# Kernel optimization log

Measured on AMD Instinct MI355X. Metric: run time of the kernel, lower is better.

The kernel has to match this reference:

```python
import jax, jax.numpy as jnp
import numpy as np

N = 50000   # nodes
E = 600000  # edges
D = 128     # embedding_dim
L = 4       # num_message_passing_steps


def setup_inputs() -> dict:
    key = jax.random.key(0)
    ks = jax.random.split(key, 5)
    x = jax.random.normal(ks[0], (N, D), dtype=jnp.float32)
    edge_index = jax.random.randint(ks[1], (2, E), 0, N, dtype=jnp.int32)
    # Per-layer params: MPNN linear (no bias), GCNConv weight + bias.
    lin_w = jax.random.normal(ks[2], (L, D, D), dtype=jnp.float32) / np.sqrt(D).astype(np.float32)
    gcn_w = jax.random.normal(ks[3], (L, D, D), dtype=jnp.float32) / np.sqrt(D).astype(np.float32)
    gcn_b = jax.random.normal(ks[4], (L, D), dtype=jnp.float32) * 0.01
    return {"x": x, "edge_index": edge_index, "lin_w": lin_w, "gcn_w": gcn_w, "gcn_b": gcn_b}


def reference(x, edge_index, lin_w, gcn_w, gcn_b):
    n = x.shape[0]
    # GCNConv defaults: add_self_loops=True, normalize=True.
    loops = jnp.arange(n, dtype=edge_index.dtype)
    src = jnp.concatenate([edge_index[0], loops])  # [E+N]
    dst = jnp.concatenate([edge_index[1], loops])  # [E+N]
    # Degree computed on dst (col) for flow='source_to_target'.
    deg = jax.ops.segment_sum(jnp.ones_like(src, dtype=x.dtype), dst, num_segments=n)
    dinv = jnp.where(deg > 0, jax.lax.rsqrt(jnp.maximum(deg, 1.0)), 0.0)
    norm = dinv[src] * dinv[dst]  # [E+N]

    for l in range(lin_w.shape[0]):
        h = x @ lin_w[l].T                 # MPNNLayer.linear (no bias)
        h = h @ gcn_w[l].T                 # GCNConv internal linear
        msgs = h[src] * norm[:, None]      # gather + normalize  [E+N, D]
        agg = jax.ops.segment_sum(msgs, dst, num_segments=n)
        x = agg + gcn_b[l]                 # GCNConv bias
        # NOTE: self.relu is `Sequential as ReLU` -> empty Sequential = identity.
    return x
```

## Files before the change

kernel.cpp:

```cpp
#include <hip/hip_runtime.h>

#define DEMB 128
#define EB 8192

typedef __attribute__((ext_vector_type(8))) _Float16 half8;
typedef __attribute__((ext_vector_type(4))) _Float16 half4;
typedef __attribute__((ext_vector_type(4))) float f32x4;

__global__ void kwc(const float* __restrict__ gcn, const float* __restrict__ lin,
                    float* __restrict__ Ms) {
  __shared__ float sa[128];
  int l = blockIdx.x >> 7, i = blockIdx.x & 127, j = threadIdx.x;
  sa[j] = gcn[((size_t)l * 128 + i) * 128 + j];
  __syncthreads();
  float acc = 0.f;
#pragma unroll 8
  for (int k = 0; k < 128; ++k) acc += sa[k] * lin[((size_t)l * 128 + k) * 128 + j];
  Ms[((size_t)l * 128 + i) * 128 + j] = acc;
}

__global__ void kst2(const float* __restrict__ Ms, const float* __restrict__ gb,
                     float* __restrict__ A1, float* __restrict__ B1,
                     float* __restrict__ v0, float* __restrict__ cb) {
  const float* M0 = Ms;
  const float* M1 = Ms + 16384;
  const float* M2 = Ms + 2 * 16384;
  const float* M3 = Ms + 3 * 16384;
  __shared__ float sa[128];
  int b = blockIdx.x, j = threadIdx.x;
  if (b < 128) {
    sa[j] = M1[b * 128 + j];
    __syncthreads();
    float acc = 0.f;
#pragma unroll 8
    for (int k = 0; k < 128; ++k) acc += sa[k] * M0[k * 128 + j];
    A1[b * 128 + j] = acc;
  } else if (b < 256) {
    int i = b - 128;
    sa[j] = M3[i * 128 + j];
    __syncthreads();
    float acc = 0.f;
#pragma unroll 8
    for (int k = 0; k < 128; ++k) acc += sa[k] * M2[k * 128 + j];
    B1[i * 128 + j] = acc;
  } else if (b == 256) {
    sa[j] = gb[j];
    __syncthreads();
    float acc = 0.f;
#pragma unroll 8
    for (int k = 0; k < 128; ++k) acc += M1[j * 128 + k] * sa[k];
    v0[j] = acc;
  } else {
    sa[j] = gb[2 * 128 + j];
    __syncthreads();
    float acc = 0.f;
#pragma unroll 8
    for (int k = 0; k < 128; ++k) acc += M3[j * 128 + k] * sa[k];
    cb[256 + j] = acc;
  }
}

__global__ void kst3(const float* __restrict__ A1, const float* __restrict__ B1,
                     const float* __restrict__ v0, const float* __restrict__ gb,
                     _Float16* __restrict__ Rh, float* __restrict__ cb) {
  __shared__ float sa[128];
  int b = blockIdx.x, j = threadIdx.x;
  if (b < 128) {
    sa[j] = B1[b * 128 + j];
    __syncthreads();
    float acc = 0.f;
#pragma unroll 8
    for (int k = 0; k < 128; ++k) acc += sa[k] * A1[k * 128 + j];
    Rh[b * 128 + j] = (_Float16)acc;
  } else if (b == 128) {
    sa[j] = v0[j];
    __syncthreads();
    float acc = 0.f;
#pragma unroll 8
    for (int k = 0; k < 128; ++k) acc += B1[j * 128 + k] * sa[k];
    cb[j] = acc;
  } else {
    sa[j] = gb[128 + j];
    __syncthreads();
    float acc = 0.f;
#pragma unroll 8
    for (int k = 0; k < 128; ++k) acc += B1[j * 128 + k] * sa[k];
    cb[128 + j] = acc;
  }
}

__global__ void khist(const int* __restrict__ ei, int* __restrict__ histG,
                      int etot, int nbB) {
  __shared__ int lh[256];
  int t = threadIdx.x;
  lh[t] = 0;
  __syncthreads();
#pragma unroll 4
  for (int j = 0; j < EB / 256; ++j) {
    int i = blockIdx.x * EB + j * 256 + t;
    if (i < etot) atomicAdd(&lh[ei[etot + i] >> 8], 1);
  }
  __syncthreads();
  histG[t * nbB + blockIdx.x] = lh[t];
}

__global__ void kbase(int* __restrict__ histG, int* __restrict__ binOff,
                      int nbB, int etot) {
  __shared__ int s[256];
  int t = threadIdx.x;
  int* row = histG + t * nbB;
  int tot = 0;
#pragma unroll 4
  for (int b = 0; b < nbB; ++b) tot += row[b];
  s[t] = tot;
  __syncthreads();
  for (int o = 1; o < 256; o <<= 1) {
    int v = (t >= o) ? s[t - o] : 0;
    __syncthreads();
    s[t] += v;
    __syncthreads();
  }
  int bstart = s[t] - tot;
  binOff[t] = bstart;
  if (t == 255) binOff[256] = etot;
  int run = bstart;
  for (int b = 0; b < nbB; ++b) {
    int v = row[b];
    row[b] = run;
    run += v;
  }
}

__global__ void kscatter(const int* __restrict__ ei, const int* __restrict__ histG,
                         int2* __restrict__ pr, int etot, int nbB) {
  __shared__ int cur[256];
  int t = threadIdx.x;
  cur[t] = histG[t * nbB + blockIdx.x];
  __syncthreads();
#pragma unroll 4
  for (int j = 0; j < EB / 256; ++j) {
    int i = blockIdx.x * EB + j * 256 + t;
    if (i < etot) {
      int src = ei[i], dst = ei[etot + i];
      int p = atomicAdd(&cur[dst >> 8], 1);
      pr[p] = make_int2(src, dst);
    }
  }
}

__global__ void kdeg2(const int2* __restrict__ pr, const int* __restrict__ binOff,
                      int* __restrict__ deg, int n) {
  __shared__ int dl[256];
  int t = threadIdx.x, b = blockIdx.x;
  dl[t] = 0;
  __syncthreads();
  int s1 = binOff[b + 1];
  for (int p = binOff[b] + t; p < s1; p += 256)
    atomicAdd(&dl[pr[p].y & 255], 1);
  __syncthreads();
  int node = (b << 8) + t;
  if (node < n) deg[node] = dl[t];
}

__global__ void kscan1(const int* __restrict__ deg, int* __restrict__ off,
                       int* __restrict__ bsum, float* __restrict__ dinv,
                       float* __restrict__ dinv2, int n) {
  __shared__ int s[256];
  int t = threadIdx.x, i = blockIdx.x * 256 + t;
  int c = 0;
  if (i < n) {
    c = deg[i];
    float dv = rsqrtf((float)(c + 1));
    dinv[i] = dv;
    dinv2[i] = dv * dv;
  }
  s[t] = c;
  __syncthreads();
  for (int o = 1; o < 256; o <<= 1) {
    int v = (t >= o) ? s[t - o] : 0;
    __syncthreads();
    s[t] += v;
    __syncthreads();
  }
  if (i < n) off[i] = s[t] - c;
  if (t == 255) bsum[blockIdx.x] = s[t];
}

__global__ void kscan2(const int* __restrict__ bsum, int* __restrict__ boff,
                       int nb, int* __restrict__ off, int n, int etot) {
  __shared__ int s[256];
  int t = threadIdx.x;
  int c = (t < nb) ? bsum[t] : 0;
  s[t] = c;
  __syncthreads();
  for (int o = 1; o < 256; o <<= 1) {
    int v = (t >= o) ? s[t - o] : 0;
    __syncthreads();
    s[t] += v;
    __syncthreads();
  }
  if (t < nb) boff[t] = s[t] - c;
  if (t == 0) off[n] = etot;
}

__global__ void kscan3(int* __restrict__ off, const int* __restrict__ boff, int n) {
  int i = blockIdx.x * 256 + threadIdx.x;
  if (i < n) off[i] += boff[i >> 8];
}

__global__ void kfill2(const int2* __restrict__ pr, const int* __restrict__ binOff,
                       const int* __restrict__ off, int* __restrict__ csr, int n) {
  __shared__ int cur[256];
  int t = threadIdx.x, b = blockIdx.x;
  int node = (b << 8) + t;
  cur[t] = (node < n) ? off[node] : 0;
  __syncthreads();
  int s1 = binOff[b + 1];
  for (int p = binOff[b] + t; p < s1; p += 256) {
    int2 e = pr[p];
    int pos = atomicAdd(&cur[e.y & 255], 1);
    csr[pos] = e.x;
  }
}

__global__ void kpre(const float* __restrict__ x, const float* __restrict__ dinv,
                     _Float16* __restrict__ xh, int n) {
  int gid = blockIdx.x * 256 + threadIdx.x;
  if (gid >= n * 32) return;
  int r = gid >> 5, c = (gid & 31) * 4;
  float d = dinv[r];
  float4 v = *(const float4*)(x + (size_t)r * DEMB + c);
  half4 o = {(_Float16)(v.x * d), (_Float16)(v.y * d), (_Float16)(v.z * d), (_Float16)(v.w * d)};
  *(half4*)(xh + (size_t)r * DEMB + c) = o;
}

template <int WITHU>
__launch_bounds__(256)
__global__ void kagg16(const _Float16* __restrict__ vin, const int* __restrict__ csr,
                       const int* __restrict__ off, const float* __restrict__ scale,
                       const float* __restrict__ dinv, const float* __restrict__ a_in,
                       float* __restrict__ u_out, float* __restrict__ a_out,
                       _Float16* __restrict__ vout, int n) {
  int node = (int)((blockIdx.x * 256u + threadIdx.x) >> 4);
  if (node >= n) return;
  int l16 = threadIdx.x & 15;
  const _Float16* base = vin + 8 * l16;
  half8 sv = *(const half8*)(base + (size_t)node * DEMB);
  float acc[8];
#pragma unroll
  for (int j = 0; j < 8; ++j) acc[j] = (float)sv[j];
  float s = WITHU ? a_in[node] : 0.f;
  int e = off[node], end = off[node + 1];
  for (; e + 8 <= end; e += 8) {
    int i0 = csr[e], i1 = csr[e + 1], i2 = csr[e + 2], i3 = csr[e + 3];
    int i4 = csr[e + 4], i5 = csr[e + 5], i6 = csr[e + 6], i7 = csr[e + 7];
    half8 r0 = *(const half8*)(base + (size_t)i0 * DEMB);
    half8 r1 = *(const half8*)(base + (size_t)i1 * DEMB);
    half8 r2 = *(const half8*)(base + (size_t)i2 * DEMB);
    half8 r3 = *(const half8*)(base + (size_t)i3 * DEMB);
    half8 r4 = *(const half8*)(base + (size_t)i4 * DEMB);
    half8 r5 = *(const half8*)(base + (size_t)i5 * DEMB);
    half8 r6 = *(const half8*)(base + (size_t)i6 * DEMB);
    half8 r7 = *(const half8*)(base + (size_t)i7 * DEMB);
    if (WITHU)
      s += a_in[i0] + a_in[i1] + a_in[i2] + a_in[i3] +
           a_in[i4] + a_in[i5] + a_in[i6] + a_in[i7];
#pragma unroll
    for (int j = 0; j < 8; ++j)
      acc[j] += ((float)r0[j] + (float)r1[j]) + ((float)r2[j] + (float)r3[j]) +
                ((float)r4[j] + (float)r5[j]) + ((float)r6[j] + (float)r7[j]);
  }
  for (; e + 4 <= end; e += 4) {
    int i0 = csr[e], i1 = csr[e + 1], i2 = csr[e + 2], i3 = csr[e + 3];
    half8 r0 = *(const half8*)(base + (size_t)i0 * DEMB);
    half8 r1 = *(const half8*)(base + (size_t)i1 * DEMB);
    half8 r2 = *(const half8*)(base + (size_t)i2 * DEMB);
    half8 r3 = *(const half8*)(base + (size_t)i3 * DEMB);
    if (WITHU) s += a_in[i0] + a_in[i1] + a_in[i2] + a_in[i3];
#pragma unroll
    for (int j = 0; j < 8; ++j)
      acc[j] += ((float)r0[j] + (float)r1[j]) + ((float)r2[j] + (float)r3[j]);
  }
  if (e < end) {
    int em = end - 1;
    int i0 = csr[e];
    int i1 = csr[min(e + 1, em)];
    int i2 = csr[min(e + 2, em)];
    float w1 = (e + 1 < end) ? 1.f : 0.f;
    float w2 = (e + 2 < end) ? 1.f : 0.f;
    half8 r0 = *(const half8*)(base + (size_t)i0 * DEMB);
    half8 r1 = *(const half8*)(base + (size_t)i1 * DEMB);
    half8 r2 = *(const half8*)(base + (size_t)i2 * DEMB);
    if (WITHU) s += a_in[i0] + w1 * a_in[i1] + w2 * a_in[i2];
#pragma unroll
    for (int j = 0; j < 8; ++j)
      acc[j] += (float)r0[j] + w1 * (float)r1[j] + w2 * (float)r2[j];
  }
  float sc = scale[node];
  half8 o;
#pragma unroll
  for (int j = 0; j < 8; ++j) o[j] = (_Float16)(acc[j] * sc);
  *(half8*)(vout + (size_t)node * DEMB + 8 * l16) = o;
  if (WITHU && l16 == 0) {
    float dv = dinv[node];
    float u = dv * s;
    u_out[node] = u;
    a_out[node] = dv * u;
  }
}

__launch_bounds__(256)
__global__ void kgemm16(const _Float16* __restrict__ y, const _Float16* __restrict__ Rh,
                        const float* __restrict__ u1, const float* __restrict__ u2,
                        const float* __restrict__ u3, const float* __restrict__ cb,
                        const float* __restrict__ b3, float* __restrict__ out, int n) {
  int t = threadIdx.x;
  int wv = t >> 6, lane = t & 63;
  int l16 = lane & 15, g = lane >> 4;
  int row0 = blockIdx.x * 128 + wv * 32;
  f32x4 acc[2][8];
#pragma unroll
  for (int w = 0; w < 2; ++w)
#pragma unroll
    for (int n8 = 0; n8 < 8; ++n8) acc[w][n8] = (f32x4){0.f, 0.f, 0.f, 0.f};

#pragma unroll
  for (int k0 = 0; k0 < 128; k0 += 32) {
    half8 a0 = *(const half8*)(y + (size_t)(row0 + l16) * DEMB + k0 + g * 8);
    half8 a1 = *(const half8*)(y + (size_t)(row0 + 16 + l16) * DEMB + k0 + g * 8);
#pragma unroll
    for (int n8 = 0; n8 < 8; ++n8) {
      half8 b = *(const half8*)(Rh + (size_t)(n8 * 16 + l16) * DEMB + k0 + g * 8);
      acc[0][n8] = __builtin_amdgcn_mfma_f32_16x16x32_f16(a0, b, acc[0][n8], 0, 0, 0);
      acc[1][n8] = __builtin_amdgcn_mfma_f32_16x16x32_f16(a1, b, acc[1][n8], 0, 0, 0);
    }
  }
#pragma unroll
  for (int n8 = 0; n8 < 8; ++n8) {
    int col = n8 * 16 + l16;
    float cA = cb[col], cB = cb[128 + col], cC = cb[256 + col], bb = b3[col];
#pragma unroll
    for (int w = 0; w < 2; ++w)
#pragma unroll
      for (int r = 0; r < 4; ++r) {
        int row = row0 + w * 16 + g * 4 + r;
        if (row < n) {
          out[(size_t)row * DEMB + col] =
              acc[w][n8][r] + u3[row] * cA + u2[row] * cB + u1[row] * cC + bb;
        }
      }
  }
}

extern "C" void kernel_launch(void* const* d_in, const int* in_sizes, int n_in,
                              void* d_out, int out_size, void* d_ws, size_t ws_size,
                              hipStream_t stream) {
  const float* x0 = (const float*)d_in[0];
  const int* ei = (const int*)d_in[1];
  const float* lin = (const float*)d_in[2];
  const float* gcn = (const float*)d_in[3];
  const float* gb = (const float*)d_in[4];
  float* out = (float*)d_out;

  int N = in_sizes[0] / DEMB;
  int E = in_sizes[1] / 2;
  int L = in_sizes[2] / (DEMB * DEMB);
  int NP = (N + 127) & ~127;
  int NBINS = (N + 255) >> 8;
  int nbB = (E + EB - 1) / EB;

  char* w = (char*)d_ws;
  auto carve = [&](size_t bytes) {
    char* p = w;
    w += (bytes + 255) & ~(size_t)255;
    return p;
  };
  float* Ms    = (float*)carve((size_t)L * DEMB * DEMB * 4);
  float* A1    = (float*)carve((size_t)DEMB * DEMB * 4);
  float* B1    = (float*)carve((size_t)DEMB * DEMB * 4);
  _Float16* Rh = (_Float16*)carve((size_t)DEMB * DEMB * 2);
  float* v0    = (float*)carve((size_t)DEMB * 4);
  float* cb    = (float*)carve((size_t)3 * DEMB * 4);
  float* dinv  = (float*)carve((size_t)N * 4);
  float* dnv2  = (float*)carve((size_t)N * 4);
  int* deg     = (int*)carve((size_t)N * 4);
  int* off     = (int*)carve((size_t)(N + 1) * 4);
  int* histG   = (int*)carve((size_t)256 * nbB * 4);
  int* binOff  = (int*)carve(257 * 4);
  int2* pr     = (int2*)carve((size_t)E * 8);
  int* bsum    = (int*)carve(256 * 4);
  int* boff    = (int*)carve(256 * 4);
  int* csr     = (int*)carve((size_t)E * 4);
  float* u1    = (float*)carve((size_t)N * 4);
  float* u2    = (float*)carve((size_t)N * 4);
  float* u3    = (float*)carve((size_t)N * 4);
  float* a1    = (float*)carve((size_t)N * 4);
  float* a2    = (float*)carve((size_t)N * 4);
  float* a3    = (float*)carve((size_t)N * 4);
  _Float16* ha = (_Float16*)carve((size_t)NP * DEMB * 2);
  _Float16* hb = (_Float16*)carve((size_t)NP * DEMB * 2);
  (void)ws_size; (void)n_in; (void)out_size;

  int nbN = (N + 255) / 256;

  kwc<<<L * DEMB, DEMB, 0, stream>>>(gcn, lin, Ms);
  kst2<<<258, DEMB, 0, stream>>>(Ms, gb, A1, B1, v0, cb);
  kst3<<<130, DEMB, 0, stream>>>(A1, B1, v0, gb, Rh, cb);

  khist<<<nbB, 256, 0, stream>>>(ei, histG, E, nbB);
  kbase<<<1, 256, 0, stream>>>(histG, binOff, nbB, E);
  kscatter<<<nbB, 256, 0, stream>>>(ei, histG, pr, E, nbB);
  kdeg2<<<NBINS, 256, 0, stream>>>(pr, binOff, deg, N);
  kscan1<<<nbN, 256, 0, stream>>>(deg, off, bsum, dinv, dnv2, N);
  kscan2<<<1, 256, 0, stream>>>(bsum, boff, nbN, off, N, E);
  kscan3<<<nbN, 256, 0, stream>>>(off, boff, N);
  kfill2<<<NBINS, 256, 0, stream>>>(pr, binOff, off, csr, N);

  kpre<<<(N * 32 + 255) / 256, 256, 0, stream>>>(x0, dinv, ha, N);
  int nbA = (N * 16 + 255) / 256;
  kagg16<1><<<nbA, 256, 0, stream>>>(ha, csr, off, dnv2, dinv, dinv, u1, a1, hb, N);
  kagg16<1><<<nbA, 256, 0, stream>>>(hb, csr, off, dnv2, dinv, a1, u2, a2, ha, N);
  kagg16<1><<<nbA, 256, 0, stream>>>(ha, csr, off, dnv2, dinv, a2, u3, a3, hb, N);
  kagg16<0><<<nbA, 256, 0, stream>>>(hb, csr, off, dinv, dinv, nullptr, nullptr, nullptr, ha, N);

  kgemm16<<<(N + 127) / 128, 256, 0, stream>>>(ha, Rh, u1, u2, u3, cb, gb + 3 * DEMB, out, N);
}
```

Before: 220.0 us.

## Fuse weight-chain kernels, pack edge pairs, and merge CSR build kernels

Replaces the three weight-composition kernels with one kernel that chains matrix-vector products per row through shared memory, removing the intermediate workspace buffers and two launches. Edge pairs are packed into a single int (src<<8 | dst low byte), which halves the bytes written and read by the scatter and fill passes. Degree counting is folded into the first scan kernel, and the final offset fix-up is folded into the fill kernel, removing two more launches. The packing assumes src fits in 24 bits, and the serial 7-step chain in one block lengthens the weight kernel's critical path.

Result: no change. 217.9 us (-1.0%).

```diff
diff --git a/kernel.cpp b/kernel.cpp
--- a/kernel.cpp
+++ b/kernel.cpp
@@ -7,85 +7,81 @@
 typedef __attribute__((ext_vector_type(4))) _Float16 half4;
 typedef __attribute__((ext_vector_type(4))) float f32x4;
 
-__global__ void kwc(const float* __restrict__ gcn, const float* __restrict__ lin,
-                    float* __restrict__ Ms) {
-  __shared__ float sa[128];
-  int l = blockIdx.x >> 7, i = blockIdx.x & 127, j = threadIdx.x;
-  sa[j] = gcn[((size_t)l * 128 + i) * 128 + j];
-  __syncthreads();
-  float acc = 0.f;
+__global__ void kweights(const float* __restrict__ gcn, const float* __restrict__ lin,
+                         const float* __restrict__ gb, _Float16* __restrict__ Rh,
+                         float* __restrict__ cb) {
+  __shared__ float va[128], vb[128];
+  int b = blockIdx.x, j = threadIdx.x;
+  const float* G0 = gcn;
+  const float* G1 = gcn + 16384;
+  const float* G2 = gcn + 2 * 16384;
+  const float* G3 = gcn + 3 * 16384;
+  const float* L0 = lin;
+  const float* L1 = lin + 16384;
+  const float* L2 = lin + 2 * 16384;
+  const float* L3 = lin + 3 * 16384;
+  float* cur = va;
+  float* nxt = vb;
+  if (b < 128) {
+    const float* seq[7] = {L3, G2, L2, G1, L1, G0, L0};
+    va[j] = G3[b * 128 + j];
+    __syncthreads();
+#pragma unroll
+    for (int s = 0; s < 7; ++s) {
+      const float* M = seq[s];
+      float acc = 0.f;
 #pragma unroll 8
-  for (int k = 0; k < 128; ++k) acc += sa[k] * lin[((size_t)l * 128 + k) * 128 + j];
-  Ms[((size_t)l * 128 + i) * 128 + j] = acc;
-}
-
-__global__ void kst2(const float* __restrict__ Ms, const float* __restrict__ gb,
-                     float* __restrict__ A1, float* __restrict__ B1,
-                     float* __restrict__ v0, float* __restrict__ cb) {
-  const float* M0 = Ms;
-  const float* M1 = Ms + 16384;
-  const float* M2 = Ms + 2 * 16384;
-  const float* M3 = Ms + 3 * 16384;
-  __shared__ float sa[128];
-  int b = blockIdx.x, j = threadIdx.x;
-  if (b < 128) {
-    sa[j] = M1[b * 128 + j];
-    __syncthreads();
-    float acc = 0.f;
+      for (int k = 0; k < 128; ++k) acc += cur[k] * M[k * 128 + j];
+      nxt[j] = acc;
+      __syncthreads();
+      float* t2 = cur; cur = nxt; nxt = t2;
+    }
+    Rh[b * 128 + j] = (_Float16)cur[j];
+  } else if (b == 128) {
+    const float* seq[6] = {L1, G1, L2, G2, L3, G3};
+    va[j] = gb[j];
+    __syncthreads();
+#pragma unroll
+    for (int s = 0; s < 6; ++s) {
+      const float* M = seq[s];
+      float acc = 0.f;
 #pragma unroll 8
-    for (int k = 0; k < 128; ++k) acc += sa[k] * M0[k * 128 + j];
-    A1[b * 128 + j] = acc;
-  } else if (b < 256) {
-    int i = b - 128;
-    sa[j] = M3[i * 128 + j];
-    __syncthreads();
-    float acc = 0.f;
+      for (int k = 0; k < 128; ++k) acc += M[j * 128 + k] * cur[k];
+      nxt[j] = acc;
+      __syncthreads();
+      float* t2 = cur; cur = nxt; nxt = t2;
+    }
+    cb[j] = cur[j];
+  } else {
+    const float* seqB[4] = {L2, G2, L3, G3};
+    va[j] = gb[128 + j];
+    __syncthreads();
+#pragma unroll
+    for (int s = 0; s < 4; ++s) {
+      const float* M = seqB[s];
+      float acc = 0.f;
 #pragma unroll 8
-    for (int k = 0; k < 128; ++k) acc += sa[k] * M2[k * 128 + j];
-    B1[i * 128 + j] = acc;
-  } else if (b == 256) {
-    sa[j] = gb[j];
-    __syncthreads();
-    float acc = 0.f;
+      for (int k = 0; k < 128; ++k) acc += M[j * 128 + k] * cur[k];
+      nxt[j] = acc;
+      __syncthreads();
+      float* t2 = cur; cur = nxt; nxt = t2;
+    }
+    cb[128 + j] = cur[j];
+    __syncthreads();
+    cur[j] = gb[256 + j];
+    __syncthreads();
+    const float* seqC[2] = {L3, G3};
+#pragma unroll
+    for (int s = 0; s < 2; ++s) {
+      const float* M = seqC[s];
+      float acc = 0.f;
 #pragma unroll 8
-    for (int k = 0; k < 128; ++k) acc += M1[j * 128 + k] * sa[k];
-    v0[j] = acc;
-  } else {
-    sa[j] = gb[2 * 128 + j];
-    __syncthreads();
-    float acc = 0.f;
-#pragma unroll 8
-    for (int k = 0; k < 128; ++k) acc += M3[j * 128 + k] * sa[k];
-    cb[256 + j] = acc;
-  }
-}
-
-__global__ void kst3(const float* __restrict__ A1, const float* __restrict__ B1,
-                     const float* __restrict__ v0, const float* __restrict__ gb,
-                     _Float16* __restrict__ Rh, float* __restrict__ cb) {
-  __shared__ float sa[128];
-  int b = blockIdx.x, j = threadIdx.x;
-  if (b < 128) {
-    sa[j] = B1[b * 128 + j];
-    __syncthreads();
-    float acc = 0.f;
-#pragma unroll 8
-    for (int k = 0; k < 128; ++k) acc += sa[k] * A1[k * 128 + j];
-    Rh[b * 128 + j] = (_Float16)acc;
-  } else if (b == 128) {
-    sa[j] = v0[j];
-    __syncthreads();
-    float acc = 0.f;
-#pragma unroll 8
-    for (int k = 0; k < 128; ++k) acc += B1[j * 128 + k] * sa[k];
-    cb[j] = acc;
-  } else {
-    sa[j] = gb[128 + j];
-    __syncthreads();
-    float acc = 0.f;
-#pragma unroll 8
-    for (int k = 0; k < 128; ++k) acc += B1[j * 128 + k] * sa[k];
-    cb[128 + j] = acc;
+      for (int k = 0; k < 128; ++k) acc += M[j * 128 + k] * cur[k];
+      nxt[j] = acc;
+      __syncthreads();
+      float* t2 = cur; cur = nxt; nxt = t2;
+    }
+    cb[256 + j] = cur[j];
   }
 }
 
@@ -124,6 +120,7 @@
   binOff[t] = bstart;
   if (t == 255) binOff[256] = etot;
   int run = bstart;
+#pragma unroll 4
   for (int b = 0; b < nbB; ++b) {
     int v = row[b];
     row[b] = run;
@@ -132,7 +129,7 @@
 }
 
 __global__ void kscatter(const int* __restrict__ ei, const int* __restrict__ histG,
-                         int2* __restrict__ pr, int etot, int nbB) {
+                         int* __restrict__ pr, int etot, int nbB) {
   __shared__ int cur[256];
   int t = threadIdx.x;
   cur[t] = histG[t * nbB + blockIdx.x];
@@ -143,33 +140,27 @@
     if (i < etot) {
       int src = ei[i], dst = ei[etot + i];
       int p = atomicAdd(&cur[dst >> 8], 1);
-      pr[p] = make_int2(src, dst);
-    }
-  }
-}
-
-__global__ void kdeg2(const int2* __restrict__ pr, const int* __restrict__ binOff,
-                      int* __restrict__ deg, int n) {
+      pr[p] = (src << 8) | (dst & 255);
+    }
+  }
+}
+
+__global__ void kscan1(const int* __restrict__ pr, const int* __restrict__ binOff,
+                       int* __restrict__ off, int* __restrict__ bsum,
+                       float* __restrict__ dinv, float* __restrict__ dinv2, int n) {
   __shared__ int dl[256];
+  __shared__ int s[256];
   int t = threadIdx.x, b = blockIdx.x;
   dl[t] = 0;
   __syncthreads();
   int s1 = binOff[b + 1];
   for (int p = binOff[b] + t; p < s1; p += 256)
-    atomicAdd(&dl[pr[p].y & 255], 1);
-  __syncthreads();
-  int node = (b << 8) + t;
-  if (node < n) deg[node] = dl[t];
-}
-
-__global__ void kscan1(const int* __restrict__ deg, int* __restrict__ off,
-                       int* __restrict__ bsum, float* __restrict__ dinv,
-                       float* __restrict__ dinv2, int n) {
-  __shared__ int s[256];
-  int t = threadIdx.x, i = blockIdx.x * 256 + t;
+    atomicAdd(&dl[pr[p] & 255], 1);
+  __syncthreads();
+  int i = b * 256 + t;
   int c = 0;
   if (i < n) {
-    c = deg[i];
+    c = dl[t];
     float dv = rsqrtf((float)(c + 1));
     dinv[i] = dv;
     dinv2[i] = dv * dv;
@@ -183,7 +174,7 @@
     __syncthreads();
   }
   if (i < n) off[i] = s[t] - c;
-  if (t == 255) bsum[blockIdx.x] = s[t];
+  if (t == 255) bsum[b] = s[t];
 }
 
 __global__ void kscan2(const int* __restrict__ bsum, int* __restrict__ boff,
@@ -203,23 +194,24 @@
   if (t == 0) off[n] = etot;
 }
 
-__global__ void kscan3(int* __restrict__ off, const int* __restrict__ boff, int n) {
-  int i = blockIdx.x * 256 + threadIdx.x;
-  if (i < n) off[i] += boff[i >> 8];
-}
-
-__global__ void kfill2(const int2* __restrict__ pr, const int* __restrict__ binOff,
-                       const int* __restrict__ off, int* __restrict__ csr, int n) {
+__global__ void kfill2(const int* __restrict__ pr, const int* __restrict__ binOff,
+                       const int* __restrict__ boff, int* __restrict__ off,
+                       int* __restrict__ csr, int n) {
   __shared__ int cur[256];
   int t = threadIdx.x, b = blockIdx.x;
   int node = (b << 8) + t;
-  cur[t] = (node < n) ? off[node] : 0;
+  int o = 0;
+  if (node < n) {
+    o = off[node] + boff[b];
+    off[node] = o;
+  }
+  cur[t] = o;
   __syncthreads();
   int s1 = binOff[b + 1];
   for (int p = binOff[b] + t; p < s1; p += 256) {
-    int2 e = pr[p];
-    int pos = atomicAdd(&cur[e.y & 255], 1);
-    csr[pos] = e.x;
+    int v = pr[p];
+    int pos = atomicAdd(&cur[v & 255], 1);
+    csr[pos] = v >> 8;
   }
 }
 
@@ -364,7 +356,6 @@
 
   int N = in_sizes[0] / DEMB;
   int E = in_sizes[1] / 2;
-  int L = in_sizes[2] / (DEMB * DEMB);
   int NP = (N + 127) & ~127;
   int NBINS = (N + 255) >> 8;
   int nbB = (E + EB - 1) / EB;
@@ -375,19 +366,14 @@
     w += (bytes + 255) & ~(size_t)255;
     return p;
   };
-  float* Ms    = (float*)carve((size_t)L * DEMB * DEMB * 4);
-  float* A1    = (float*)carve((size_t)DEMB * DEMB * 4);
-  float* B1    = (float*)carve((size_t)DEMB * DEMB * 4);
   _Float16* Rh = (_Float16*)carve((size_t)DEMB * DEMB * 2);
-  float* v0    = (float*)carve((size_t)DEMB * 4);
   float* cb    = (float*)carve((size_t)3 * DEMB * 4);
   float* dinv  = (float*)carve((size_t)N * 4);
   float* dnv2  = (float*)carve((size_t)N * 4);
-  int* deg     = (int*)carve((size_t)N * 4);
   int* off     = (int*)carve((size_t)(N + 1) * 4);
   int* histG   = (int*)carve((size_t)256 * nbB * 4);
   int* binOff  = (int*)carve(257 * 4);
-  int2* pr     = (int2*)carve((size_t)E * 8);
+  int* pr      = (int*)carve((size_t)E * 4);
   int* bsum    = (int*)carve(256 * 4);
   int* boff    = (int*)carve(256 * 4);
   int* csr     = (int*)carve((size_t)E * 4);
@@ -401,20 +387,14 @@
   _Float16* hb = (_Float16*)carve((size_t)NP * DEMB * 2);
   (void)ws_size; (void)n_in; (void)out_size;
 
-  int nbN = (N + 255) / 256;
-
-  kwc<<<L * DEMB, DEMB, 0, stream>>>(gcn, lin, Ms);
-  kst2<<<258, DEMB, 0, stream>>>(Ms, gb, A1, B1, v0, cb);
-  kst3<<<130, DEMB, 0, stream>>>(A1, B1, v0, gb, Rh, cb);
+  kweights<<<130, DEMB, 0, stream>>>(gcn, lin, gb, Rh, cb);
 
   khist<<<nbB, 256, 0, stream>>>(ei, histG, E, nbB);
   kbase<<<1, 256, 0, stream>>>(histG, binOff, nbB, E);
   kscatter<<<nbB, 256, 0, stream>>>(ei, histG, pr, E, nbB);
-  kdeg2<<<NBINS, 256, 0, stream>>>(pr, binOff, deg, N);
-  kscan1<<<nbN, 256, 0, stream>>>(deg, off, bsum, dinv, dnv2, N);
-  kscan2<<<1, 256, 0, stream>>>(bsum, boff, nbN, off, N, E);
-  kscan3<<<nbN, 256, 0, stream>>>(off, boff, N);
-  kfill2<<<NBINS, 256, 0, stream>>>(pr, binOff, off, csr, N);
+  kscan1<<<NBINS, 256, 0, stream>>>(pr, binOff, off, bsum, dinv, dnv2, N);
+  kscan2<<<1, 256, 0, stream>>>(bsum, boff, NBINS, off, N, E);
+  kfill2<<<NBINS, 256, 0, stream>>>(pr, binOff, boff, off, csr, N);
 
   kpre<<<(N * 32 + 255) / 256, 256, 0, stream>>>(x0, dinv, ha, N);
   int nbA = (N * 16 + 255) / 256;
```
